# Optimization experiments

Hardware: AMD Instinct MI355X
Metric: run time of the kernel (lower is better)

The kernel has to match this reference:

```python
import jax, jax.numpy as jnp
import numpy as np
import math

WINDOW_SIZE = 11
SIGMA = 1.5
C3 = 0.0001


def _make_window(window_size=WINDOW_SIZE, sigma=SIGMA):
    # 1D gaussian, normalized, then outer product -> [1,1,K,K] (OIHW)
    xs = np.arange(window_size, dtype=np.float64)
    g = np.exp(-((xs - window_size // 2) ** 2) / (2.0 * sigma ** 2))
    g = g / g.sum()
    w2d = np.outer(g, g).astype(np.float32)
    return jnp.asarray(w2d)[None, None, :, :]


def setup_inputs() -> dict:
    key = jax.random.key(0)
    k1, k2 = jax.random.split(key)
    B, C, H, W = 32, 1, 512, 512
    input1 = jax.random.normal(k1, (B, C, H, W), dtype=jnp.float32)
    input2 = jax.random.normal(k2, (B, C, H, W), dtype=jnp.float32)
    window = _make_window()
    return {"input1": input1, "input2": input2, "window": window}


def _conv_valid(x, window):
    # x: [N,1,H,W], window: [1,1,K,K], channel=1 so groups=1 is exact
    return jax.lax.conv_general_dilated(
        x, window, window_strides=(1, 1), padding="VALID",
        dimension_numbers=("NCHW", "OIHW", "NCHW"))


def reference(input1, input2, window):
    B = input1.shape[0]
    # Fuse the five gaussian box-filters into one conv over a stacked batch
    stacked = jnp.concatenate(
        [input1, input2, input1 * input1, input2 * input2, input1 * input2],
        axis=0)  # [5B,1,H,W]
    filt = _conv_valid(stacked, window)  # [5B,1,H',W']
    mu1, mu2, e11, e22, e12 = (filt[i * B:(i + 1) * B] for i in range(5))
    sigma1_sq = e11 - mu1 * mu1
    sigma2_sq = e22 - mu2 * mu2
    sigma12 = e12 - mu1 * mu2
    s = (sigma12 + C3) / (jnp.sqrt(jnp.abs(sigma1_sq)) * jnp.sqrt(jnp.abs(sigma2_sq)) + C3)
    return jnp.mean(s)
```

## Files before the change

kernel.cpp:

```cpp
#include <hip/hip_runtime.h>
#include <math.h>

#define KW 11
#define HALO 10
#define TY 32
#define BATCH 32
#define HH 512
#define WW 512
#define OH 502
#define OW 502
#define NSX 8
#define WPB 2
#define NBX 4
#define NBY 16
#define NWAVE (BATCH * NBY * NSX)
#define C3V 1.0e-4f
#define SW 80

typedef float v2f __attribute__((ext_vector_type(2)));

static __device__ __forceinline__ float rfl(float x) {
    return __int_as_float(__builtin_amdgcn_readfirstlane(__float_as_int(x)));
}

__global__ __launch_bounds__(128) void ssim_strip_kernel(
    const float* __restrict__ in1,
    const float* __restrict__ in2,
    const float* __restrict__ win,
    double* __restrict__ partials)
{
    __shared__ v2f sh[WPB][KW][SW];

    const int t = threadIdx.x;
    const int wid = t >> 6;
    const int lane = t & 63;
    const int strip = blockIdx.x * WPB + wid;
    const int x0 = strip * 64;
    const int y0 = blockIdx.y * TY;
    const int img = blockIdx.z;

    const int nx = min(64, OW - x0);
    const int ny = min(TY, OH - y0);

    v2f gp[6];
    {
        const float c = sqrtf(win[5 * KW + 5]);
        #pragma unroll
        for (int i = 0; i < 6; ++i) {
            const float w = rfl(win[i * KW + 5] / c);
            gp[i] = (v2f){w, w};
        }
    }
    #define GW(j) gp[(j) <= 5 ? (j) : 10 - (j)]

    const float maskf = (lane < nx) ? 1.f : 0.f;
    const bool stager = lane < 40;
    const int scol = min(x0 + 2 * lane, WW - 2);
    const float* b1 = in1 + (size_t)img * HH * WW;
    const float* b2 = in2 + (size_t)img * HH * WW;

    v2f* const mysh = &sh[wid][0][0];

    v2f vaA, vbA, vaB, vbB;

#define LOADR_A(q) { const int rq = min(y0 + (q), HH - 1);            \
    vaA = *(const v2f*)(b1 + (size_t)rq * WW + scol);                 \
    vbA = *(const v2f*)(b2 + (size_t)rq * WW + scol); }
#define LOADR_B(q) { const int rq = min(y0 + (q), HH - 1);            \
    vaB = *(const v2f*)(b1 + (size_t)rq * WW + scol);                 \
    vbB = *(const v2f*)(b2 + (size_t)rq * WW + scol); }
#define WRITES_A(slot) { if (stager)                                   \
    *(float4*)&mysh[(slot) * SW + 2 * lane] =                          \
        make_float4(vaA.x, vbA.x, vaA.y, vbA.y); }
#define WRITES_B(slot) { if (stager)                                   \
    *(float4*)&mysh[(slot) * SW + 2 * lane] =                          \
        make_float4(vaB.x, vbB.x, vaB.y, vbB.y); }
#define RDWIN(slot) { const v2f* rp = mysh + (slot) * SW + lane;       \
    _Pragma("unroll") for (int j = 0; j < KW; ++j) W[j] = rp[j]; }

    v2f accab[KW], accsq[KW];
    float acc4[KW];
    #pragma unroll
    for (int i = 0; i < KW; ++i) {
        accab[i] = (v2f){0.f, 0.f}; accsq[i] = (v2f){0.f, 0.f}; acc4[i] = 0.f;
    }

    v2f W[KW];
    double tsum = 0.0;

    LOADR_A(0);
    WRITES_A(0);
    RDWIN(0);
    LOADR_A(1);
    LOADR_B(2);

#define PHASE(p, SET) {                                                 \
    const int yr = cbase + (p);                                         \
        \
    v2f hab = (v2f){0.f, 0.f}, hsq = (v2f){0.f, 0.f};                   \
    float h4 = 0.f;                                                     \
    _Pragma("unroll")                                                   \
    for (int j = 0; j < KW; ++j) {                                      \
        const v2f ab = W[j];                                            \
        const v2f g = GW(j);                                            \
        const v2f gab = g * ab;                                         \
        hab = __builtin_elementwise_fma(g, ab, hab);                    \
        hsq = __builtin_elementwise_fma(gab, ab, hsq);                  \
        h4 = fmaf(gab.x, ab.y, h4);                                     \
    }                                                                   \
             \
    WRITES_##SET(((p) + 1) % KW);                                       \
                                \
    RDWIN(((p) + 1) % KW);                                              \
                                 \
    LOADR_##SET(yr + 3);                                                \
      \
                       \
    _Pragma("unroll")                                                   \
    for (int r = 0; r < KW; ++r) {                                      \
        const int j = (r - (p) + KW) % KW;                              \
        const v2f g = GW(10 - j);                                       \
        if (j == 10) {                                                  \
            accab[r] = g * hab;                                         \
            accsq[r] = g * hsq;                                         \
            acc4[r] = g.x * h4;                                         \
        } else {                                                        \
            accab[r] = __builtin_elementwise_fma(g, hab, accab[r]);     \
            accsq[r] = __builtin_elementwise_fma(g, hsq, accsq[r]);     \
            acc4[r] = fmaf(g.x, h4, acc4[r]);                           \
        }                                                               \
    }                                                                   \
      \
    if (yr >= HALO) {                                                   \
        const v2f mu = accab[(p)];                                      \
        const v2f sq = __builtin_elementwise_fma(-mu, mu, accsq[(p)]);  \
        const float s12 = fmaf(-mu.x, mu.y, acc4[(p)]);                 \
        const float den = __builtin_amdgcn_sqrtf(fabsf(sq.x * sq.y)) + C3V; \
        const float s = (s12 + C3V) * __builtin_amdgcn_rcpf(den);       \
        const float m = ((yr - HALO) < ny) ? maskf : 0.f;               \
        csum = fmaf(s, m, csum);                                        \
    }                                                                   \
}

    for (int c = 0; c < 4; ++c) {
        const int cbase = c * KW;
        float csum = 0.f;
        PHASE(0, A) PHASE(1, B) PHASE(2, A) PHASE(3, B) PHASE(4, A)
        PHASE(5, B) PHASE(6, A) PHASE(7, B) PHASE(8, A) PHASE(9, B)
        PHASE(10, A)
        tsum += (double)csum;
        { v2f tmp;
          tmp = vaA; vaA = vaB; vaB = tmp;
          tmp = vbA; vbA = vbB; vbB = tmp; }
    }
#undef PHASE
#undef LOADR_A
#undef LOADR_B
#undef WRITES_A
#undef WRITES_B
#undef RDWIN
#undef GW

    #pragma unroll
    for (int off = 32; off > 0; off >>= 1)
        tsum += __shfl_down(tsum, off, 64);
    if (lane == 0) {
        const int bid = (img * NBY + blockIdx.y) * NSX + strip;
        partials[bid] = tsum;
    }
}

__global__ __launch_bounds__(256) void ssim_reduce_kernel(
    const double* __restrict__ partials, float* __restrict__ out)
{
    __shared__ double sred[4];
    double s = 0.0;
    for (int i = threadIdx.x; i < NWAVE; i += 256) s += partials[i];
    #pragma unroll
    for (int off = 32; off > 0; off >>= 1)
        s += __shfl_down(s, off, 64);
    const int wid = threadIdx.x >> 6;
    const int lane = threadIdx.x & 63;
    if (lane == 0) sred[wid] = s;
    __syncthreads();
    if (threadIdx.x == 0) {
        const double total = sred[0] + sred[1] + sred[2] + sred[3];
        out[0] = (float)(total / ((double)BATCH * OH * OW));
    }
}

extern "C" void kernel_launch(void* const* d_in, const int* in_sizes, int n_in,
                              void* d_out, int out_size, void* d_ws, size_t ws_size,
                              hipStream_t stream) {
    const float* in1 = (const float*)d_in[0];
    const float* in2 = (const float*)d_in[1];
    const float* win = (const float*)d_in[2];
    float* out = (float*)d_out;
    double* partials = (double*)d_ws;

    dim3 grid(NBX, NBY, BATCH);
    dim3 block(WPB * 64);
    ssim_strip_kernel<<<grid, block, 0, stream>>>(in1, in2, win, partials);
    ssim_reduce_kernel<<<1, 256, 0, stream>>>(partials, out);
}
```

Before: 46.98 us.

## Double-buffer LDS window reads and deepen global-load prefetch by one row

The strip kernel now keeps two register copies of the horizontal window. It reads the next row's window from LDS before computing the current row's horizontal filter, which hides LDS latency behind the FMA chain. Staging writes now run two rows ahead and global loads four rows ahead instead of one and three. This costs 22 more VGPRs for the second window buffer, which may lower occupancy. Writing LDS within a single wave without a barrier relies on wave-level ordering.

```diff
diff --git a/kernel.cpp b/kernel.cpp
--- a/kernel.cpp
+++ b/kernel.cpp
@@ -75,8 +75,8 @@
 #define WRITES_B(slot) { if (stager)                                   \
     *(float4*)&mysh[(slot) * SW + 2 * lane] =                          \
         make_float4(vaB.x, vbB.x, vaB.y, vbB.y); }
-#define RDWIN(slot) { const v2f* rp = mysh + (slot) * SW + lane;       \
-    _Pragma("unroll") for (int j = 0; j < KW; ++j) W[j] = rp[j]; }
+#define RDWIN(slot, Warr) { const v2f* rp = mysh + (slot) * SW + lane; \
+    _Pragma("unroll") for (int j = 0; j < KW; ++j) Warr[j] = rp[j]; }
 
     v2f accab[KW], accsq[KW];
     float acc4[KW];
@@ -85,23 +85,24 @@
         accab[i] = (v2f){0.f, 0.f}; accsq[i] = (v2f){0.f, 0.f}; acc4[i] = 0.f;
     }
 
-    v2f W[KW];
+    v2f W0[KW], W1[KW];
     double tsum = 0.0;
 
-    LOADR_A(0);
-    WRITES_A(0);
-    RDWIN(0);
-    LOADR_A(1);
-    LOADR_B(2);
-
-#define PHASE(p, SET) {                                                 \
+    LOADR_A(0); WRITES_A(0); RDWIN(0, W0);
+    LOADR_B(1); WRITES_B(1);
+    LOADR_A(2);
+    LOADR_B(3);
+
+#define PHASE(p, S, Wc, Wn) {                                           \
     const int yr = cbase + (p);                                         \
-        \
+       \
+    RDWIN(((p) + 1) % KW, Wn);                                          \
+                \
     v2f hab = (v2f){0.f, 0.f}, hsq = (v2f){0.f, 0.f};                   \
     float h4 = 0.f;                                                     \
     _Pragma("unroll")                                                   \
     for (int j = 0; j < KW; ++j) {                                      \
-        const v2f ab = W[j];                                            \
+        const v2f ab = Wc[j];                                           \
         const v2f g = GW(j);                                            \
         const v2f gab = g * ab;                                         \
         hab = __builtin_elementwise_fma(g, ab, hab);                    \
@@ -109,11 +110,9 @@
         h4 = fmaf(gab.x, ab.y, h4);                                     \
     }                                                                   \
              \
-    WRITES_##SET(((p) + 1) % KW);                                       \
-                                \
-    RDWIN(((p) + 1) % KW);                                              \
+    WRITES_##S(((p) + 2) % KW);                                         \
                                  \
-    LOADR_##SET(yr + 3);                                                \
+    LOADR_##S(yr + 4);                                                  \
       \
                        \
     _Pragma("unroll")                                                   \
@@ -145,13 +144,18 @@
     for (int c = 0; c < 4; ++c) {
         const int cbase = c * KW;
         float csum = 0.f;
-        PHASE(0, A) PHASE(1, B) PHASE(2, A) PHASE(3, B) PHASE(4, A)
-        PHASE(5, B) PHASE(6, A) PHASE(7, B) PHASE(8, A) PHASE(9, B)
-        PHASE(10, A)
+        PHASE(0, A, W0, W1) PHASE(1, B, W1, W0)
+        PHASE(2, A, W0, W1) PHASE(3, B, W1, W0)
+        PHASE(4, A, W0, W1) PHASE(5, B, W1, W0)
+        PHASE(6, A, W0, W1) PHASE(7, B, W1, W0)
+        PHASE(8, A, W0, W1) PHASE(9, B, W1, W0)
+        PHASE(10, A, W0, W1)
         tsum += (double)csum;
         { v2f tmp;
           tmp = vaA; vaA = vaB; vaB = tmp;
           tmp = vbA; vbA = vbB; vbB = tmp; }
+        #pragma unroll
+        for (int j = 0; j < KW; ++j) { v2f tmp = W0[j]; W0[j] = W1[j]; W1[j] = tmp; }
     }
 #undef PHASE
 #undef LOADR_A
```

New measurement: 47.55 us. No clear change (+1.2%).
